# Kernel optimization log

Hardware: AMD Instinct MI355X
Metric: run time of the kernel (lower is better)

Reference implementation:

```python
import jax, jax.numpy as jnp
import numpy as np

N_NODES = 100000
EPS = 1e-12  # F.normalize eps


def _glorot(key, shape):
    fan_in, fan_out = shape[0], shape[1]
    lim = (6.0 / (fan_in + fan_out)) ** 0.5
    return jax.random.uniform(key, shape, jnp.float32, -lim, lim)


def setup_inputs() -> dict:
    key = jax.random.key(0)
    ks = jax.random.split(key, 8)
    d_in, d_hid, d_out = 128, 128, 64
    x = jax.random.normal(ks[0], (N_NODES, d_in), jnp.float32)
    edge_index = jax.random.randint(ks[1], (2, 1600000), 0, N_NODES, jnp.int32)
    return {
        "x": x,
        "edge_index": edge_index,
        "Wl1": _glorot(ks[2], (d_in, d_hid)),
        "Wr1": _glorot(ks[3], (d_in, d_hid)),
        "b1": jnp.zeros((d_hid,), jnp.float32),
        "Wl2": _glorot(ks[4], (d_hid, d_out)),
        "Wr2": _glorot(ks[5], (d_hid, d_out)),
        "b2": jnp.zeros((d_out,), jnp.float32),
    }


def _sage_conv(x, src, dst, Wl, Wr, b):
    # gather source-node features per edge, max-aggregate onto destinations
    msgs = x[src]                                   # [E, d]
    agg = jax.ops.segment_max(msgs, dst, num_segments=N_NODES)
    # PyG scatter-max leaves 0 for nodes with no incoming edges
    agg = jnp.where(jnp.isneginf(agg), 0.0, agg)    # [N, d]
    out = agg @ Wl + x @ Wr + b                     # lin_l(aggr) + lin_r(root)
    # normalize=True -> L2 normalize rows (F.normalize semantics)
    norm = jnp.maximum(jnp.linalg.norm(out, axis=-1, keepdims=True), EPS)
    return out / norm


def reference(x, edge_index, Wl1, Wr1, b1, Wl2, Wr2, b2):
    src, dst = edge_index[0], edge_index[1]
    # dropout p=0.9 is identity in eval mode
    h = jax.nn.relu(_sage_conv(x, src, dst, Wl1, Wr1, b1))
    return _sage_conv(h, src, dst, Wl2, Wr2, b2)
```

## Files before the change

kernel.cpp:

```cpp
#include <hip/hip_runtime.h>
#include <math.h>

typedef __attribute__((ext_vector_type(8))) short short8;
typedef __attribute__((ext_vector_type(4))) float floatx4;

static __device__ __forceinline__ ushort f32_to_bf16_rne(float f) {
  union { float f; unsigned int i; } c;
  c.f = f;
  unsigned int lsb = (c.i >> 16) & 1u;
  c.i += 0x7fffu + lsb;
  return (ushort)(c.i >> 16);
}
static __device__ __forceinline__ float bf16_lo(unsigned int v) {
  union { unsigned int i; float f; } c;
  c.i = v << 16;
  return c.f;
}
static __device__ __forceinline__ float bf16_hi(unsigned int v) {
  union { unsigned int i; float f; } c;
  c.i = v & 0xffff0000u;
  return c.f;
}


#define NBLK 256

__global__ __launch_bounds__(256) void binhist_kernel(const int* __restrict__ dst,
                                                      int* __restrict__ bh, int E, int EBLK,
                                                      int NBUCKET) {
  __shared__ int h[256];
  int t = threadIdx.x, blk = blockIdx.x;
  h[t] = 0;
  __syncthreads();
  int e0 = blk * EBLK, e1 = min(E, e0 + EBLK);
  for (int e = e0 + t; e < e1; e += 256) atomicAdd(&h[dst[e] >> 9], 1);
  __syncthreads();
  if (t < NBUCKET) bh[t * NBLK + blk] = h[t];
}

__global__ void scan1_kernel(const int* __restrict__ counts, int* __restrict__ offsets,
                             int* __restrict__ tileSums, int N) {
  __shared__ int sd[256];
  int t = threadIdx.x;
  int base = blockIdx.x * 1024 + t * 4;
  int v[4];
#pragma unroll
  for (int i = 0; i < 4; i++) v[i] = (base + i < N) ? counts[base + i] : 0;
  int s = v[0] + v[1] + v[2] + v[3];
  sd[t] = s;
  __syncthreads();
  int acc = s;
  for (int off = 1; off < 256; off <<= 1) {
    int add = (t >= off) ? sd[t - off] : 0;
    __syncthreads();
    acc += add;
    sd[t] = acc;
    __syncthreads();
  }
  int run = acc - s;
#pragma unroll
  for (int i = 0; i < 4; i++) {
    if (base + i < N) offsets[base + i] = run;
    run += v[i];
  }
  if (t == 255) tileSums[blockIdx.x] = acc;
}

__global__ void scan2_kernel(int* __restrict__ tileSums, int nT) {
  __shared__ int sd[128];
  int t = threadIdx.x;
  int v = (t < nT) ? tileSums[t] : 0;
  sd[t] = v;
  __syncthreads();
  int acc = v;
  for (int off = 1; off < 128; off <<= 1) {
    int add = (t >= off) ? sd[t - off] : 0;
    __syncthreads();
    acc += add;
    sd[t] = acc;
    __syncthreads();
  }
  if (t < nT) tileSums[t] = acc - v;
}

__global__ void scan3_nc_kernel(int* __restrict__ offsets, const int* __restrict__ tileSums,
                                int N) {
  int i = blockIdx.x * 256 + threadIdx.x;
  if (i >= N) return;
  offsets[i] += tileSums[i >> 10];
}

__global__ __launch_bounds__(256) void binscatter_kernel(const int* __restrict__ src,
                                                         const int* __restrict__ dst,
                                                         const int* __restrict__ bhOff,
                                                         int2* __restrict__ binned, int E,
                                                         int EBLK, int NBUCKET) {
  __shared__ int cur[256];
  int t = threadIdx.x, blk = blockIdx.x;
  if (t < NBUCKET) cur[t] = bhOff[t * NBLK + blk];
  __syncthreads();
  int e0 = blk * EBLK, e1 = min(E, e0 + EBLK);
  for (int e = e0 + t; e < e1; e += 256) {
    int d = dst[e];
    int pos = atomicAdd(&cur[d >> 9], 1);
    binned[pos] = make_int2(src[e], d);
  }
}

__global__ __launch_bounds__(256) void bucket_build_kernel(
    const int2* __restrict__ binned, const int* __restrict__ bhOff, int* __restrict__ counts,
    int* __restrict__ offsets, int* __restrict__ csr, int N, int E, int NBUCKET) {
  __shared__ int h[512];
  __shared__ int lofs[512];
  __shared__ int cur[512];
  __shared__ int sd[256];
  int b = blockIdx.x, t = threadIdx.x;
  int S = bhOff[b * NBLK];
  int Send = (b + 1 < NBUCKET) ? bhOff[(b + 1) * NBLK] : E;
  h[t] = 0;
  h[t + 256] = 0;
  __syncthreads();
  for (int e = S + t; e < Send; e += 256) atomicAdd(&h[binned[e].y & 511], 1);
  __syncthreads();
  int h0 = h[2 * t], h1 = h[2 * t + 1];
  int s = h0 + h1;
  sd[t] = s;
  __syncthreads();
  int acc = s;
  for (int off = 1; off < 256; off <<= 1) {
    int add = (t >= off) ? sd[t - off] : 0;
    __syncthreads();
    acc += add;
    sd[t] = acc;
    __syncthreads();
  }
  int run = acc - s;
  lofs[2 * t] = run;
  lofs[2 * t + 1] = run + h0;
  __syncthreads();
  int node0 = b * 512;
#pragma unroll
  for (int i = 0; i < 2; i++) {
    int l = t + i * 256;
    int node = node0 + l;
    if (node < N) {
      counts[node] = h[l];
      offsets[node] = S + lofs[l];
    }
    cur[l] = S + lofs[l];
  }
  __syncthreads();
  for (int e = S + t; e < Send; e += 256) {
    int2 r = binned[e];
    int pos = atomicAdd(&cur[r.y & 511], 1);
    csr[pos] = r.x;
  }
}


__global__ void f32_to_bf16_kernel(const float* __restrict__ in, ushort* __restrict__ out, int n) {
  int i = (blockIdx.x * 256 + threadIdx.x) * 8;
  if (i >= n) return;
  float4 a = *(const float4*)(in + i);
  float4 b = *(const float4*)(in + i + 4);
  union { ushort u[8]; short8 v; } r;
  r.u[0] = f32_to_bf16_rne(a.x); r.u[1] = f32_to_bf16_rne(a.y);
  r.u[2] = f32_to_bf16_rne(a.z); r.u[3] = f32_to_bf16_rne(a.w);
  r.u[4] = f32_to_bf16_rne(b.x); r.u[5] = f32_to_bf16_rne(b.y);
  r.u[6] = f32_to_bf16_rne(b.z); r.u[7] = f32_to_bf16_rne(b.w);
  *(short8*)(out + i) = r.v;
}

__global__ void wt_conv_kernel(const float* __restrict__ W, ushort* __restrict__ WT, int K, int C) {
  int idx = blockIdx.x * 256 + threadIdx.x;
  if (idx >= K * C) return;
  int k = idx / C, c = idx % C;
  WT[(size_t)c * K + k] = f32_to_bf16_rne(W[idx]);
}


__global__ void agg_max_bf16_kernel(const ushort* __restrict__ feat, const int* __restrict__ csr,
                                    const int* __restrict__ offsets, const int* __restrict__ counts,
                                    unsigned int* __restrict__ aggb, int N) {
  int lane = threadIdx.x & 63;
  int node = (blockIdx.x * blockDim.x + threadIdx.x) >> 6;
  if (node >= N) return;
  const unsigned int* fu = (const unsigned int*)feat;
  int start = offsets[node];
  int deg = counts[node];
  float m0 = 0.0f, m1 = 0.0f;
  if (deg > 0) {
    m0 = -INFINITY;
    m1 = -INFINITY;
    int e = 0;
    for (; e + 4 <= deg; e += 4) {
      int s0 = csr[start + e + 0];
      int s1 = csr[start + e + 1];
      int s2 = csr[start + e + 2];
      int s3 = csr[start + e + 3];
      unsigned int v0 = fu[(size_t)s0 * 64 + lane];
      unsigned int v1 = fu[(size_t)s1 * 64 + lane];
      unsigned int v2 = fu[(size_t)s2 * 64 + lane];
      unsigned int v3 = fu[(size_t)s3 * 64 + lane];
      m0 = fmaxf(m0, fmaxf(fmaxf(bf16_lo(v0), bf16_lo(v1)), fmaxf(bf16_lo(v2), bf16_lo(v3))));
      m1 = fmaxf(m1, fmaxf(fmaxf(bf16_hi(v0), bf16_hi(v1)), fmaxf(bf16_hi(v2), bf16_hi(v3))));
    }
    for (; e < deg; e++) {
      unsigned int v = fu[(size_t)csr[start + e] * 64 + lane];
      m0 = fmaxf(m0, bf16_lo(v));
      m1 = fmaxf(m1, bf16_hi(v));
    }
  }
  unsigned int res = (__float_as_uint(m0) >> 16) | (__float_as_uint(m1) & 0xffff0000u);
  aggb[(size_t)node * 64 + lane] = res;
}


template <int DOUT, bool RELU, bool OUTBF16>
__global__ __launch_bounds__(256) void gemm_mfma_kernel(
    const ushort* __restrict__ A, const ushort* __restrict__ X, const ushort* __restrict__ WlT,
    const ushort* __restrict__ WrT, const float* __restrict__ bias, void* __restrict__ outp,
    int N) {
  constexpr int D = 128;
  constexpr int NCT = DOUT / 16;
  int t = threadIdx.x;
  int lane = t & 63;
  int wid = t >> 6;
  int l16 = lane & 15;
  int lk = lane >> 4;
  int rowbase = blockIdx.x * 128 + wid * 32;

  floatx4 acc[2][NCT];
#pragma unroll
  for (int rt = 0; rt < 2; rt++)
#pragma unroll
    for (int ct = 0; ct < NCT; ct++) acc[rt][ct] = (floatx4){0.f, 0.f, 0.f, 0.f};

  int ra = rowbase + l16;       if (ra > N - 1) ra = N - 1;
  int rb = rowbase + 16 + l16;  if (rb > N - 1) rb = N - 1;
  const ushort* pA0 = A + (size_t)ra * D;
  const ushort* pA1 = A + (size_t)rb * D;
  const ushort* pX0 = X + (size_t)ra * D;
  const ushort* pX1 = X + (size_t)rb * D;

#pragma unroll
  for (int kc = 0; kc < 4; kc++) {
    int ko = kc * 32 + lk * 8;
    short8 a0 = *(const short8*)(pA0 + ko);
    short8 a1 = *(const short8*)(pA1 + ko);
    short8 x0 = *(const short8*)(pX0 + ko);
    short8 x1 = *(const short8*)(pX1 + ko);
#pragma unroll
    for (int ct = 0; ct < NCT; ct++) {
      int c = ct * 16 + l16;
      short8 bl = *(const short8*)(WlT + (size_t)c * D + ko);
      short8 br = *(const short8*)(WrT + (size_t)c * D + ko);
      acc[0][ct] = __builtin_amdgcn_mfma_f32_16x16x32_bf16(a0, bl, acc[0][ct], 0, 0, 0);
      acc[0][ct] = __builtin_amdgcn_mfma_f32_16x16x32_bf16(x0, br, acc[0][ct], 0, 0, 0);
      acc[1][ct] = __builtin_amdgcn_mfma_f32_16x16x32_bf16(a1, bl, acc[1][ct], 0, 0, 0);
      acc[1][ct] = __builtin_amdgcn_mfma_f32_16x16x32_bf16(x1, br, acc[1][ct], 0, 0, 0);
    }
  }

  float bb[NCT];
#pragma unroll
  for (int ct = 0; ct < NCT; ct++) bb[ct] = bias[ct * 16 + l16];
#pragma unroll
  for (int rt = 0; rt < 2; rt++)
#pragma unroll
    for (int ct = 0; ct < NCT; ct++)
#pragma unroll
      for (int r = 0; r < 4; r++) acc[rt][ct][r] += bb[ct];

#pragma unroll
  for (int rt = 0; rt < 2; rt++) {
#pragma unroll
    for (int r = 0; r < 4; r++) {
      float ss = 0.f;
#pragma unroll
      for (int ct = 0; ct < NCT; ct++) ss += acc[rt][ct][r] * acc[rt][ct][r];
      ss += __shfl_xor(ss, 1);
      ss += __shfl_xor(ss, 2);
      ss += __shfl_xor(ss, 4);
      ss += __shfl_xor(ss, 8);
      float inv = 1.0f / fmaxf(sqrtf(ss), 1e-12f);
      int n = rowbase + rt * 16 + lk * 4 + r;
      if (n < N) {
#pragma unroll
        for (int ct = 0; ct < NCT; ct++) {
          float v = acc[rt][ct][r] * inv;
          if (RELU) v = fmaxf(v, 0.f);
          size_t o = (size_t)n * DOUT + ct * 16 + l16;
          if (OUTBF16)
            ((ushort*)outp)[o] = f32_to_bf16_rne(v);
          else
            ((float*)outp)[o] = v;
        }
      }
    }
  }
}


extern "C" void kernel_launch(void* const* d_in, const int* in_sizes, int n_in, void* d_out,
                              int out_size, void* d_ws, size_t ws_size, hipStream_t stream) {
  const float* x = (const float*)d_in[0];
  const int* ei = (const int*)d_in[1];
  const float* Wl1 = (const float*)d_in[2];
  const float* Wr1 = (const float*)d_in[3];
  const float* b1 = (const float*)d_in[4];
  const float* Wl2 = (const float*)d_in[5];
  const float* Wr2 = (const float*)d_in[6];
  const float* b2 = (const float*)d_in[7];
  float* out = (float*)d_out;

  const int E = in_sizes[1] / 2;
  const int N = in_sizes[0] / 128;
  const int D = 128;

  const int* src = ei;
  const int* dst = ei + E;

  char* w = (char*)d_ws;
  size_t off = 0;
  auto alloc = [&](size_t bytes) {
    void* p = w + off;
    off = (off + bytes + 511) & ~((size_t)511);
    return p;
  };
  const int NBUCKET = (N + 511) >> 9;
  const int M = NBUCKET * NBLK;
  int* bh = (int*)alloc((size_t)M * 4);
  int* tileSums = (int*)alloc(512);
  int* counts = (int*)alloc((size_t)N * 4);
  int* offsets = (int*)alloc((size_t)N * 4);
  int2* binned = (int2*)alloc((size_t)E * 8);
  int* csr = (int*)alloc((size_t)E * 4);
  ushort* xb = (ushort*)alloc((size_t)N * D * 2);
  ushort* aggb = (ushort*)alloc((size_t)N * D * 2);
  ushort* hb = (ushort*)alloc((size_t)N * D * 2);
  ushort* WlT1 = (ushort*)alloc(128 * 128 * 2);
  ushort* WrT1 = (ushort*)alloc(128 * 128 * 2);
  ushort* WlT2 = (ushort*)alloc(128 * 64 * 2);
  ushort* WrT2 = (ushort*)alloc(128 * 64 * 2);
  (void)ws_size;

  const int EBLK = (E + NBLK - 1) / NBLK;
  const int nTiles = (M + 1023) / 1024;

  binhist_kernel<<<NBLK, 256, 0, stream>>>(dst, bh, E, EBLK, NBUCKET);
  scan1_kernel<<<nTiles, 256, 0, stream>>>(bh, bh, tileSums, M);
  scan2_kernel<<<1, 128, 0, stream>>>(tileSums, nTiles);
  scan3_nc_kernel<<<(M + 255) / 256, 256, 0, stream>>>(bh, tileSums, M);
  binscatter_kernel<<<NBLK, 256, 0, stream>>>(src, dst, bh, binned, E, EBLK, NBUCKET);
  bucket_build_kernel<<<NBUCKET, 256, 0, stream>>>(binned, bh, counts, offsets, csr, N, E,
                                                   NBUCKET);

  f32_to_bf16_kernel<<<(N * D / 8 + 255) / 256, 256, 0, stream>>>(x, xb, N * D);
  wt_conv_kernel<<<(128 * 128 + 255) / 256, 256, 0, stream>>>(Wl1, WlT1, 128, 128);
  wt_conv_kernel<<<(128 * 128 + 255) / 256, 256, 0, stream>>>(Wr1, WrT1, 128, 128);
  wt_conv_kernel<<<(128 * 64 + 255) / 256, 256, 0, stream>>>(Wl2, WlT2, 128, 64);
  wt_conv_kernel<<<(128 * 64 + 255) / 256, 256, 0, stream>>>(Wr2, WrT2, 128, 64);

  const int nbGemm = (N + 127) / 128;

  agg_max_bf16_kernel<<<(N * 64 + 255) / 256, 256, 0, stream>>>(xb, csr, offsets, counts,
                                                                (unsigned int*)aggb, N);
  gemm_mfma_kernel<128, true, true>
      <<<nbGemm, 256, 0, stream>>>(aggb, xb, WlT1, WrT1, b1, hb, N);

  agg_max_bf16_kernel<<<(N * 64 + 255) / 256, 256, 0, stream>>>(hb, csr, offsets, counts,
                                                                (unsigned int*)aggb, N);
  gemm_mfma_kernel<64, false, false>
      <<<nbGemm, 256, 0, stream>>>(aggb, hb, WlT2, WrT2, b2, out, N);
}
```

Baseline: 396.7 us.

## Split node features into column-slice layout so each aggregation pass gathers from one slice

```diff
diff --git a/kernel.cpp b/kernel.cpp
--- a/kernel.cpp
+++ b/kernel.cpp
@@ -33,7 +33,7 @@
   h[t] = 0;
   __syncthreads();
   int e0 = blk * EBLK, e1 = min(E, e0 + EBLK);
-  for (int e = e0 + t; e < e1; e += 256) atomicAdd(&h[dst[e] >> 9], 1);
+  for (int e = e0 + t; e < e1; e += 256) atomicAdd(&h[__builtin_nontemporal_load(dst + e) >> 9], 1);
   __syncthreads();
   if (t < NBUCKET) bh[t * NBLK + blk] = h[t];
 }
@@ -101,9 +101,10 @@
   __syncthreads();
   int e0 = blk * EBLK, e1 = min(E, e0 + EBLK);
   for (int e = e0 + t; e < e1; e += 256) {
-    int d = dst[e];
+    int d = __builtin_nontemporal_load(dst + e);
+    int s = __builtin_nontemporal_load(src + e);
     int pos = atomicAdd(&cur[d >> 9], 1);
-    binned[pos] = make_int2(src[e], d);
+    binned[pos] = make_int2(s, d);
   }
 }
 
@@ -120,7 +121,10 @@
   h[t] = 0;
   h[t + 256] = 0;
   __syncthreads();
-  for (int e = S + t; e < Send; e += 256) atomicAdd(&h[binned[e].y & 511], 1);
+  for (int e = S + t; e < Send; e += 256) {
+    long long rv = __builtin_nontemporal_load((const long long*)binned + e);
+    atomicAdd(&h[(int)(rv >> 32) & 511], 1);
+  }
   __syncthreads();
   int h0 = h[2 * t], h1 = h[2 * t + 1];
   int s = h0 + h1;
@@ -151,24 +155,22 @@
   }
   __syncthreads();
   for (int e = S + t; e < Send; e += 256) {
-    int2 r = binned[e];
-    int pos = atomicAdd(&cur[r.y & 511], 1);
-    csr[pos] = r.x;
-  }
-}
-
-
-__global__ void f32_to_bf16_kernel(const float* __restrict__ in, ushort* __restrict__ out, int n) {
-  int i = (blockIdx.x * 256 + threadIdx.x) * 8;
-  if (i >= n) return;
-  float4 a = *(const float4*)(in + i);
-  float4 b = *(const float4*)(in + i + 4);
-  union { ushort u[8]; short8 v; } r;
-  r.u[0] = f32_to_bf16_rne(a.x); r.u[1] = f32_to_bf16_rne(a.y);
-  r.u[2] = f32_to_bf16_rne(a.z); r.u[3] = f32_to_bf16_rne(a.w);
-  r.u[4] = f32_to_bf16_rne(b.x); r.u[5] = f32_to_bf16_rne(b.y);
-  r.u[6] = f32_to_bf16_rne(b.z); r.u[7] = f32_to_bf16_rne(b.w);
-  *(short8*)(out + i) = r.v;
+    long long rv = __builtin_nontemporal_load((const long long*)binned + e);
+    int pos = atomicAdd(&cur[(int)(rv >> 32) & 511], 1);
+    csr[pos] = (int)(rv & 0xffffffff);
+  }
+}
+
+
+__global__ void x_to_xt_kernel(const float* __restrict__ x, unsigned int* __restrict__ xt, int N) {
+  int idx = blockIdx.x * 256 + threadIdx.x;
+  if (idx >= N * 64) return;
+  int n = idx >> 6, q = idx & 63;
+  int g = q >> 3, j = q & 7;
+  float a = x[(size_t)n * 128 + q * 2];
+  float b = x[(size_t)n * 128 + q * 2 + 1];
+  unsigned int r = (unsigned int)f32_to_bf16_rne(a) | ((unsigned int)f32_to_bf16_rne(b) << 16);
+  xt[(size_t)g * N * 8 + (size_t)n * 8 + j] = r;
 }
 
 __global__ void wt_conv_kernel(const float* __restrict__ W, ushort* __restrict__ WT, int K, int C) {
@@ -179,13 +181,21 @@
 }
 
 
-__global__ void agg_max_bf16_kernel(const ushort* __restrict__ feat, const int* __restrict__ csr,
-                                    const int* __restrict__ offsets, const int* __restrict__ counts,
-                                    unsigned int* __restrict__ aggb, int N) {
-  int lane = threadIdx.x & 63;
-  int node = (blockIdx.x * blockDim.x + threadIdx.x) >> 6;
+__global__ __launch_bounds__(256) void agg_max_xt_kernel(
+    const unsigned int* __restrict__ xt, const int* __restrict__ csr,
+    const int* __restrict__ offsets, const int* __restrict__ counts,
+    unsigned int* __restrict__ aggt, int N) {
+  int t = threadIdx.x;
+  int b = blockIdx.x;
+  int g = b & 7;
+  int chunk = b >> 3;
+  int lane = t & 63;
+  int wid = t >> 6;
+  int slot = lane >> 3;
+  int j = lane & 7;
+  int node = chunk * 32 + wid * 8 + slot;
   if (node >= N) return;
-  const unsigned int* fu = (const unsigned int*)feat;
+  const unsigned int* base = xt + (size_t)g * N * 8;
   int start = offsets[node];
   int deg = counts[node];
   float m0 = 0.0f, m1 = 0.0f;
@@ -194,25 +204,25 @@
     m1 = -INFINITY;
     int e = 0;
     for (; e + 4 <= deg; e += 4) {
-      int s0 = csr[start + e + 0];
-      int s1 = csr[start + e + 1];
-      int s2 = csr[start + e + 2];
-      int s3 = csr[start + e + 3];
-      unsigned int v0 = fu[(size_t)s0 * 64 + lane];
-      unsigned int v1 = fu[(size_t)s1 * 64 + lane];
-      unsigned int v2 = fu[(size_t)s2 * 64 + lane];
-      unsigned int v3 = fu[(size_t)s3 * 64 + lane];
+      int s0 = __builtin_nontemporal_load(csr + start + e + 0);
+      int s1 = __builtin_nontemporal_load(csr + start + e + 1);
+      int s2 = __builtin_nontemporal_load(csr + start + e + 2);
+      int s3 = __builtin_nontemporal_load(csr + start + e + 3);
+      unsigned int v0 = base[(size_t)s0 * 8 + j];
+      unsigned int v1 = base[(size_t)s1 * 8 + j];
+      unsigned int v2 = base[(size_t)s2 * 8 + j];
+      unsigned int v3 = base[(size_t)s3 * 8 + j];
       m0 = fmaxf(m0, fmaxf(fmaxf(bf16_lo(v0), bf16_lo(v1)), fmaxf(bf16_lo(v2), bf16_lo(v3))));
       m1 = fmaxf(m1, fmaxf(fmaxf(bf16_hi(v0), bf16_hi(v1)), fmaxf(bf16_hi(v2), bf16_hi(v3))));
     }
     for (; e < deg; e++) {
-      unsigned int v = fu[(size_t)csr[start + e] * 64 + lane];
+      unsigned int v = base[(size_t)__builtin_nontemporal_load(csr + start + e) * 8 + j];
       m0 = fmaxf(m0, bf16_lo(v));
       m1 = fmaxf(m1, bf16_hi(v));
     }
   }
   unsigned int res = (__float_as_uint(m0) >> 16) | (__float_as_uint(m1) & 0xffff0000u);
-  aggb[(size_t)node * 64 + lane] = res;
+  aggt[(size_t)g * N * 8 + (size_t)node * 8 + j] = res;
 }
 
 
@@ -238,18 +248,19 @@
 
   int ra = rowbase + l16;       if (ra > N - 1) ra = N - 1;
   int rb = rowbase + 16 + l16;  if (rb > N - 1) rb = N - 1;
-  const ushort* pA0 = A + (size_t)ra * D;
-  const ushort* pA1 = A + (size_t)rb * D;
-  const ushort* pX0 = X + (size_t)ra * D;
-  const ushort* pX1 = X + (size_t)rb * D;
+
+  size_t sliceN = (size_t)N * 16;
+  int goff = (lk & 1) * 8;
 
 #pragma unroll
   for (int kc = 0; kc < 4; kc++) {
+    int g = kc * 2 + (lk >> 1);
+    size_t sbase = (size_t)g * sliceN + goff;
+    short8 a0 = *(const short8*)(A + sbase + (size_t)ra * 16);
+    short8 a1 = *(const short8*)(A + sbase + (size_t)rb * 16);
+    short8 x0 = *(const short8*)(X + sbase + (size_t)ra * 16);
+    short8 x1 = *(const short8*)(X + sbase + (size_t)rb * 16);
     int ko = kc * 32 + lk * 8;
-    short8 a0 = *(const short8*)(pA0 + ko);
-    short8 a1 = *(const short8*)(pA1 + ko);
-    short8 x0 = *(const short8*)(pX0 + ko);
-    short8 x1 = *(const short8*)(pX1 + ko);
 #pragma unroll
     for (int ct = 0; ct < NCT; ct++) {
       int c = ct * 16 + l16;
@@ -290,11 +301,11 @@
         for (int ct = 0; ct < NCT; ct++) {
           float v = acc[rt][ct][r] * inv;
           if (RELU) v = fmaxf(v, 0.f);
-          size_t o = (size_t)n * DOUT + ct * 16 + l16;
-          if (OUTBF16)
-            ((ushort*)outp)[o] = f32_to_bf16_rne(v);
-          else
-            ((float*)outp)[o] = v;
+          if (OUTBF16) {
+            ((ushort*)outp)[(size_t)ct * sliceN + (size_t)n * 16 + l16] = f32_to_bf16_rne(v);
+          } else {
+            ((float*)outp)[(size_t)n * DOUT + ct * 16 + l16] = v;
+          }
         }
       }
     }
@@ -336,9 +347,9 @@
   int* offsets = (int*)alloc((size_t)N * 4);
   int2* binned = (int2*)alloc((size_t)E * 8);
   int* csr = (int*)alloc((size_t)E * 4);
-  ushort* xb = (ushort*)alloc((size_t)N * D * 2);
-  ushort* aggb = (ushort*)alloc((size_t)N * D * 2);
-  ushort* hb = (ushort*)alloc((size_t)N * D * 2);
+  ushort* xbt = (ushort*)alloc((size_t)N * D * 2);
+  ushort* aggt = (ushort*)alloc((size_t)N * D * 2);
+  ushort* hbt = (ushort*)alloc((size_t)N * D * 2);
   ushort* WlT1 = (ushort*)alloc(128 * 128 * 2);
   ushort* WrT1 = (ushort*)alloc(128 * 128 * 2);
   ushort* WlT2 = (ushort*)alloc(128 * 64 * 2);
@@ -356,21 +367,22 @@
   bucket_build_kernel<<<NBUCKET, 256, 0, stream>>>(binned, bh, counts, offsets, csr, N, E,
                                                    NBUCKET);
 
-  f32_to_bf16_kernel<<<(N * D / 8 + 255) / 256, 256, 0, stream>>>(x, xb, N * D);
+  x_to_xt_kernel<<<(N * 64 + 255) / 256, 256, 0, stream>>>(x, (unsigned int*)xbt, N);
   wt_conv_kernel<<<(128 * 128 + 255) / 256, 256, 0, stream>>>(Wl1, WlT1, 128, 128);
   wt_conv_kernel<<<(128 * 128 + 255) / 256, 256, 0, stream>>>(Wr1, WrT1, 128, 128);
   wt_conv_kernel<<<(128 * 64 + 255) / 256, 256, 0, stream>>>(Wl2, WlT2, 128, 64);
   wt_conv_kernel<<<(128 * 64 + 255) / 256, 256, 0, stream>>>(Wr2, WrT2, 128, 64);
 
+  const int nbAgg = ((N + 31) / 32) * 8;
   const int nbGemm = (N + 127) / 128;
 
-  agg_max_bf16_kernel<<<(N * 64 + 255) / 256, 256, 0, stream>>>(xb, csr, offsets, counts,
-                                                                (unsigned int*)aggb, N);
+  agg_max_xt_kernel<<<nbAgg, 256, 0, stream>>>((const unsigned int*)xbt, csr, offsets, counts,
+                                               (unsigned int*)aggt, N);
   gemm_mfma_kernel<128, true, true>
-      <<<nbGemm, 256, 0, stream>>>(aggb, xb, WlT1, WrT1, b1, hb, N);
-
-  agg_max_bf16_kernel<<<(N * 64 + 255) / 256, 256, 0, stream>>>(hb, csr, offsets, counts,
-                                                                (unsigned int*)aggb, N);
+      <<<nbGemm, 256, 0, stream>>>(aggt, xbt, WlT1, WrT1, b1, hbt, N);
+
+  agg_max_xt_kernel<<<nbAgg, 256, 0, stream>>>((const unsigned int*)hbt, csr, offsets, counts,
+                                               (unsigned int*)aggt, N);
   gemm_mfma_kernel<64, false, false>
-      <<<nbGemm, 256, 0, stream>>>(aggb, hb, WlT2, WrT2, b2, out, N);
-}
+      <<<nbGemm, 256, 0, stream>>>(aggt, hbt, WlT2, WrT2, b2, out, N);
+}
```

Measured after the change: 541.2 us. +36.4%, slower.
